# Performance work log

Measured on AMD Instinct MI355X. Metric: run time of the kernel, lower is better.

The kernel has to match this reference:

```python
import jax, jax.numpy as jnp
import numpy as np


def _gru_cell(x, h, W_ih, W_hh, b_ih, b_hh):
    # PyTorch GRUCell math, gate order (r, z, n) along the 3*H axis.
    gi = x @ W_ih.T + b_ih          # [B, 3H]
    gh = h @ W_hh.T + b_hh          # [B, 3H]
    i_r, i_z, i_n = jnp.split(gi, 3, axis=-1)
    h_r, h_z, h_n = jnp.split(gh, 3, axis=-1)
    r = jax.nn.sigmoid(i_r + h_r)
    z = jax.nn.sigmoid(i_z + h_z)
    n = jnp.tanh(i_n + r * h_n)
    return (1.0 - z) * n + z * h


def setup_inputs() -> dict:
    key = jax.random.key(0)
    ks = jax.random.split(key, 12)
    V, E, H, L, B, T = 16000, 512, 1024, 2, 32, 64
    s = 0.05  # small init scale to keep gates unsaturated
    return {
        "hidden": jax.random.normal(ks[0], (L, B, H), jnp.float32),
        "embed": jax.random.normal(ks[1], (V, E), jnp.float32) * s,
        "W_ih0": jax.random.normal(ks[2], (3 * H, E), jnp.float32) * s,
        "W_hh0": jax.random.normal(ks[3], (3 * H, H), jnp.float32) * s,
        "b_ih0": jax.random.normal(ks[4], (3 * H,), jnp.float32) * s,
        "b_hh0": jax.random.normal(ks[5], (3 * H,), jnp.float32) * s,
        "W_ih1": jax.random.normal(ks[6], (3 * H, H), jnp.float32) * s,
        "W_hh1": jax.random.normal(ks[7], (3 * H, H), jnp.float32) * s,
        "b_ih1": jax.random.normal(ks[8], (3 * H,), jnp.float32) * s,
        "b_hh1": jax.random.normal(ks[9], (3 * H,), jnp.float32) * s,
        "W_out": jax.random.normal(ks[10], (V, H), jnp.float32) * s,
        "b_out": jax.random.normal(ks[11], (V,), jnp.float32) * s,
        "max_len": 64,
        "batch_size": 32,
    }


def reference(hidden, embed, W_ih0, W_hh0, b_ih0, b_hh0,
              W_ih1, W_hh1, b_ih1, b_hh1, W_out, b_out,
              max_len, batch_size):
    # target=None path: teacher_forcing_ratio forced to 0 -> greedy argmax decode.
    tok0 = jnp.zeros((batch_size,), jnp.int32)  # curr_token starts at zeros

    def step(carry, _):
        h, tok = carry                      # h: [2, B, H], tok: [B] int32
        x = embed[tok]                      # [B, E] embedding lookup
        h0 = _gru_cell(x, h[0], W_ih0, W_hh0, b_ih0, b_hh0)
        h1 = _gru_cell(h0, h[1], W_ih1, W_hh1, b_ih1, b_hh1)
        logits = h1 @ W_out.T + b_out       # [B, V]
        tok_next = jnp.argmax(logits, axis=1).astype(jnp.int32)
        return (jnp.stack([h0, h1]), tok_next), logits

    (_, _), outputs = jax.lax.scan(step, (hidden, tok0), None, length=max_len)
    return outputs  # [max_len, B, V]
```

## Files before the change

### kernel.cpp

```cpp
#include <hip/hip_runtime.h>
#include <stdint.h>

#define V_ 16000
#define E_ 512
#define H_ 1024
#define B_ 32
#define T_ 64
#define NG_ 3072
#define NR_ 6144
#define IHB_ 96
#define TPAD_ 8

typedef float f32x4 __attribute__((ext_vector_type(4)));
typedef unsigned long long u64;

__device__ __forceinline__ unsigned int fkey(float f) {
    unsigned int u = __float_as_uint(f);
    return (u & 0x80000000u) ? ~u : (u | 0x80000000u);
}

__global__ void init_kernel(const float* __restrict__ hidden,
                            float* __restrict__ h0, float* __restrict__ h1,
                            u64* __restrict__ tokpk) {
    int idx = blockIdx.x * blockDim.x + threadIdx.x;
    if (idx < B_ * H_) {
        h0[idx] = hidden[idx];
        h1[idx] = hidden[B_ * H_ + idx];
    }
    if (idx < T_ * B_ * TPAD_) tokpk[idx] = 0ull;
}

__device__ __forceinline__ void gemm_core(
    const float* wp, const float* ap,
    int nch, float* lds, int tid, float acc[4][4])
{
    const int k4s = tid & 15;
    const int r   = tid >> 4;
    const int dW  = (r << 6) + ((k4s ^ (r & 7)) << 2);
    const int ks   = tid >> 6;
    const int lane = tid & 63;
    const int vg = lane >> 3, bg = lane & 7;

    f32x4 tW = *(const f32x4*)(wp + (k4s << 2));
    f32x4 tA = *(const f32x4*)(ap + (k4s << 2));
    *(f32x4*)&lds[dW] = tW;
    *(f32x4*)&lds[2048 + dW] = tA;
    __syncthreads();

    int cur = 0;
    for (int c = 0; c < nch; c++) {
        if (c + 1 < nch) {
            const int nko = (c + 1) << 6;
            tW = *(const f32x4*)(wp + nko + (k4s << 2));
            tA = *(const f32x4*)(ap + nko + (k4s << 2));
        }
        const float* Wb = &lds[cur * 4096];
        const float* Ab = &lds[cur * 4096 + 2048];
        #pragma unroll
        for (int kk = 0; kk < 2; kk++) {
            const int k4 = ks * 2 + kk;
            f32x4 ww[4], ha[4];
            #pragma unroll
            for (int vi = 0; vi < 4; vi++)
                ww[vi] = *(const f32x4*)&Wb[((vg + 8*vi) << 6) + ((k4 ^ vg) << 2)];
            #pragma unroll
            for (int j = 0; j < 4; j++)
                ha[j] = *(const f32x4*)&Ab[((bg + 8*j) << 6) + ((k4 ^ bg) << 2)];
            #pragma unroll
            for (int vi = 0; vi < 4; vi++)
                #pragma unroll
                for (int j = 0; j < 4; j++)
                    acc[vi][j] += ww[vi].x*ha[j].x + ww[vi].y*ha[j].y
                                + ww[vi].z*ha[j].z + ww[vi].w*ha[j].w;
        }
        if (c + 1 < nch) {
            float* Wo = &lds[(cur ^ 1) * 4096];
            *(f32x4*)&Wo[dW] = tW;
            *(f32x4*)&Wo[2048 + dW] = tA;
        }
        __syncthreads();
        cur ^= 1;
    }
}

__device__ __forceinline__ void ks_reduce(float* lds, int tid,
                                          float acc[4][4], float tv[16])
{
    const int ks = tid >> 6, lane = tid & 63;
    float* dst = &lds[(ks * 64 + lane) * 17];
    #pragma unroll
    for (int vi = 0; vi < 4; vi++)
        #pragma unroll
        for (int j = 0; j < 4; j++) dst[vi*4 + j] = acc[vi][j];
    __syncthreads();
    if (tid < 64) {
        #pragma unroll
        for (int c = 0; c < 16; c++) {
            float s = 0.f;
            #pragma unroll
            for (int k = 0; k < 8; k++) s += lds[(k*64 + tid)*17 + c];
            tv[c] = s;
        }
    }
}

__global__ __launch_bounds__(512) void gemm_gru(
    const float* __restrict__ Wih, const float* __restrict__ Whh, int Kih,
    const float* __restrict__ xbase, int xld,
    const float* __restrict__ embed, const u64* __restrict__ tokprev,
    int t, int tmode,
    const float* __restrict__ hprev,
    float* __restrict__ gbuf)
{
    __shared__ float lds[8704];
    const int tid = threadIdx.x;
    const int blk = blockIdx.x;
    const int r = tid >> 4;

    const float *wp, *ap;
    int nch;
    if (blk < IHB_) {
        const int n0 = blk * 32;
        wp = Wih + (size_t)(n0 + r) * Kih;
        if (tmode) {
            int tok = 0;
            if (t > 0)
                tok = (int)(0xFFFFFFFFu -
                            (unsigned)(tokprev[(size_t)r * TPAD_] & 0xFFFFFFFFull));
            ap = embed + (size_t)tok * Kih;
        } else {
            ap = xbase + (size_t)r * xld;
        }
        nch = Kih >> 6;
    } else {
        const int n0 = (blk - IHB_) * 32;
        wp = Whh + (size_t)(n0 + r) * H_;
        ap = hprev + (size_t)r * H_;
        nch = H_ >> 6;
    }

    float acc[4][4] = {};
    gemm_core(wp, ap, nch, lds, tid, acc);
    float tv[16];
    ks_reduce(lds, tid, acc, tv);
    if (tid < 64) {
        const int vgr = tid >> 3, bgr = tid & 7;
        const int nout0 = blk * 32;
        #pragma unroll
        for (int vi = 0; vi < 4; vi++)
            #pragma unroll
            for (int j = 0; j < 4; j++)
                gbuf[(size_t)(bgr + 8*j) * NR_ + nout0 + vgr + 8*vi] = tv[vi*4+j];
    }
}

__global__ __launch_bounds__(256) void combine_kernel(
    const float* __restrict__ gbuf,
    const float* __restrict__ bih, const float* __restrict__ bhh,
    const float* __restrict__ hprev, float* __restrict__ hnew)
{
    const int idx = blockIdx.x * 256 + threadIdx.x;
    const int b = idx >> 10, i = idx & 1023;
    const float* gb = gbuf + (size_t)b * NR_;
    const float gir = gb[i],        giz = gb[H_ + i],        gin = gb[2*H_ + i];
    const float ghr = gb[NG_ + i],  ghz = gb[NG_ + H_ + i],  ghn = gb[NG_ + 2*H_ + i];
    const float Sr = gir + ghr + bih[i] + bhh[i];
    const float Sz = giz + ghz + bih[H_ + i] + bhh[H_ + i];
    const float rr = 1.f / (1.f + expf(-Sr));
    const float zz = 1.f / (1.f + expf(-Sz));
    const float nn = tanhf(gin + bih[2*H_ + i] + rr * (ghn + bhh[2*H_ + i]));
    const float hp = hprev[(size_t)b * H_ + i];
    hnew[(size_t)b * H_ + i] = (1.f - zz) * nn + zz * hp;
}

__global__ __launch_bounds__(512) void logits_kernel(
    const float* __restrict__ h1, const float* __restrict__ Wout,
    const float* __restrict__ bout, float* __restrict__ out_t,
    u64* __restrict__ tokpk_t)
{
    __shared__ float lds[10272];
    const int tid = threadIdx.x;
    const int r = tid >> 4;
    const int v0 = blockIdx.x * 32;
    const float* wp = Wout + (size_t)(v0 + r) * H_;
    const float* ap = h1 + (size_t)r * H_;

    float acc[4][4] = {};
    gemm_core(wp, ap, H_ >> 6, lds, tid, acc);
    float tv[16];
    ks_reduce(lds, tid, acc, tv);

    float* totl = lds + 8704;
    u64*   am   = (u64*)(lds + 8704 + 1056);
    if (tid < 64) {
        const int vgr = tid >> 3, bgr = tid & 7;
        #pragma unroll
        for (int vi = 0; vi < 4; vi++) {
            const float bo = bout[v0 + vgr + 8*vi];
            #pragma unroll
            for (int j = 0; j < 4; j++) tv[vi*4+j] += bo;
        }
        #pragma unroll
        for (int vi = 0; vi < 4; vi++)
            #pragma unroll
            for (int j = 0; j < 4; j++)
                totl[(bgr + 8*j) * 33 + vgr + 8*vi] = tv[vi*4+j];
        #pragma unroll
        for (int j = 0; j < 4; j++) {
            u64 best = 0ull;
            #pragma unroll
            for (int vi = 0; vi < 4; vi++) {
                const int v = v0 + vgr + 8*vi;
                u64 p = ((u64)fkey(tv[vi*4+j]) << 32)
                      | (u64)(0xFFFFFFFFu - (unsigned)v);
                best = p > best ? p : best;
            }
            am[(bgr + 8*j) * 8 + vgr] = best;
        }
    }
    __syncthreads();
    if (tid < 64) {
        const int b = tid >> 1, half = tid & 1;
        #pragma unroll
        for (int q = 0; q < 4; q++) {
            f32x4 o;
            o.x = totl[b*33 + half*16 + q*4 + 0];
            o.y = totl[b*33 + half*16 + q*4 + 1];
            o.z = totl[b*33 + half*16 + q*4 + 2];
            o.w = totl[b*33 + half*16 + q*4 + 3];
            __builtin_nontemporal_store(
                o, (f32x4*)(out_t + (size_t)b * V_ + v0 + half*16 + q*4));
        }
    }
    if (tid < 32) {
        u64 best = 0ull;
        #pragma unroll
        for (int q = 0; q < 8; q++) {
            u64 p = am[tid*8 + q];
            best = p > best ? p : best;
        }
        atomicMax(&tokpk_t[(size_t)tid * TPAD_], best);
    }
}

extern "C" void kernel_launch(void* const* d_in, const int* in_sizes, int n_in,
                              void* d_out, int out_size, void* d_ws, size_t ws_size,
                              hipStream_t stream) {
    const float* hidden = (const float*)d_in[0];
    const float* embed  = (const float*)d_in[1];
    const float* Wih0   = (const float*)d_in[2];
    const float* Whh0   = (const float*)d_in[3];
    const float* bih0   = (const float*)d_in[4];
    const float* bhh0   = (const float*)d_in[5];
    const float* Wih1   = (const float*)d_in[6];
    const float* Whh1   = (const float*)d_in[7];
    const float* bih1   = (const float*)d_in[8];
    const float* bhh1   = (const float*)d_in[9];
    const float* Wout   = (const float*)d_in[10];
    const float* bout   = (const float*)d_in[11];
    float* out = (float*)d_out;

    const int BH = B_ * H_;
    float* ws = (float*)d_ws;
    float* h0buf = ws;
    float* h1buf = ws + 2 * BH;
    float* gbuf  = ws + 4 * BH;
    u64* tokpk = (u64*)(ws + 4 * BH + B_ * NR_);

    init_kernel<<<128, 256, 0, stream>>>(hidden, h0buf, h1buf, tokpk);

    for (int t = 0; t < T_; t++) {
        const int rp = t & 1, wp = (t + 1) & 1;
        const u64* tokprev = tokpk + (size_t)(t > 0 ? t - 1 : 0) * B_ * TPAD_;

        gemm_gru<<<NR_ / 32, 512, 0, stream>>>(
            Wih0, Whh0, E_, nullptr, 0, embed, tokprev, t, 1,
            h0buf + (size_t)rp * BH, gbuf);
        combine_kernel<<<128, 256, 0, stream>>>(
            gbuf, bih0, bhh0, h0buf + (size_t)rp * BH, h0buf + (size_t)wp * BH);

        gemm_gru<<<NR_ / 32, 512, 0, stream>>>(
            Wih1, Whh1, H_, h0buf + (size_t)wp * BH, H_, embed, tokprev, 0,
            0, h1buf + (size_t)rp * BH, gbuf);
        combine_kernel<<<128, 256, 0, stream>>>(
            gbuf, bih1, bhh1, h1buf + (size_t)rp * BH, h1buf + (size_t)wp * BH);

        logits_kernel<<<V_ / 32, 512, 0, stream>>>(
            h1buf + (size_t)wp * BH, Wout, bout,
            out + (size_t)t * B_ * V_, tokpk + (size_t)t * B_ * TPAD_);
    }
}
```

Before: 4.360 ms.

## Split GRU gate GEMM K dimension across two block slices, deepen prefetch

The gate GEMM grid is doubled so each block handles half of the K dimension, writing partial sums to two gbuf slices that combine_kernel adds together. The point is more parallelism: only 192 blocks ran before on a GPU with many CUs. Separately, gemm_core now keeps two chunks in flight in registers ahead of the LDS double buffer, which hides more global-load latency. The costs are extra workspace, extra partial-sum traffic in combine, and higher register pressure.

```diff
diff --git a/kernel.cpp b/kernel.cpp
--- a/kernel.cpp
+++ b/kernel.cpp
@@ -9,6 +9,7 @@
 #define NG_ 3072
 #define NR_ 6144
 #define IHB_ 96
+#define TB_ 192
 #define TPAD_ 8
 
 typedef float f32x4 __attribute__((ext_vector_type(4)));
@@ -40,22 +41,18 @@
     const int ks   = tid >> 6;
     const int lane = tid & 63;
     const int vg = lane >> 3, bg = lane & 7;
-
-    f32x4 tW = *(const f32x4*)(wp + (k4s << 2));
-    f32x4 tA = *(const f32x4*)(ap + (k4s << 2));
-    *(f32x4*)&lds[dW] = tW;
-    *(f32x4*)&lds[2048 + dW] = tA;
-    __syncthreads();
-
-    int cur = 0;
-    for (int c = 0; c < nch; c++) {
-        if (c + 1 < nch) {
-            const int nko = (c + 1) << 6;
-            tW = *(const f32x4*)(wp + nko + (k4s << 2));
-            tA = *(const f32x4*)(ap + nko + (k4s << 2));
-        }
-        const float* Wb = &lds[cur * 4096];
-        const float* Ab = &lds[cur * 4096 + 2048];
+    float* lds0 = lds;
+    float* lds1 = lds + 4096;
+
+    auto ldW = [&](int c) { return *(const f32x4*)(wp + (c << 6) + (k4s << 2)); };
+    auto ldA = [&](int c) { return *(const f32x4*)(ap + (c << 6) + (k4s << 2)); };
+    auto stb = [&](float* b, f32x4 w, f32x4 a) {
+        *(f32x4*)&b[dW] = w;
+        *(f32x4*)&b[2048 + dW] = a;
+    };
+    auto compute = [&](const float* b) {
+        const float* Wb = b;
+        const float* Ab = b + 2048;
         #pragma unroll
         for (int kk = 0; kk < 2; kk++) {
             const int k4 = ks * 2 + kk;
@@ -73,13 +70,27 @@
                     acc[vi][j] += ww[vi].x*ha[j].x + ww[vi].y*ha[j].y
                                 + ww[vi].z*ha[j].z + ww[vi].w*ha[j].w;
         }
-        if (c + 1 < nch) {
-            float* Wo = &lds[(cur ^ 1) * 4096];
-            *(f32x4*)&Wo[dW] = tW;
-            *(f32x4*)&Wo[2048 + dW] = tA;
-        }
+    };
+
+    { f32x4 w0 = ldW(0), a0 = ldA(0); stb(lds0, w0, a0); }
+    f32x4 wA = ldW(1), aA = ldA(1);
+    f32x4 wB = ldW(2), aB = ldA(2);
+    __syncthreads();
+
+    for (int c = 0; c < nch; c += 2) {
+        f32x4 wN = wA, aN = aA;
+        if (c + 3 < nch) { wN = ldW(c + 3); aN = ldA(c + 3); }
+        compute(lds0);
+        if (c + 1 < nch) stb(lds1, wA, aA);
         __syncthreads();
-        cur ^= 1;
+        if (c + 1 >= nch) break;
+        wA = wN; aA = aN;
+        f32x4 wM = wB, aM = aB;
+        if (c + 4 < nch) { wM = ldW(c + 4); aM = ldA(c + 4); }
+        compute(lds1);
+        if (c + 2 < nch) stb(lds0, wB, aB);
+        __syncthreads();
+        wB = wM; aB = aM;
     }
 }
 
@@ -114,11 +125,13 @@
 {
     __shared__ float lds[8704];
     const int tid = threadIdx.x;
-    const int blk = blockIdx.x;
+    const int blk0 = blockIdx.x;
+    const int kslice = blk0 >= TB_ ? 1 : 0;
+    const int blk = blk0 - kslice * TB_;
     const int r = tid >> 4;
 
     const float *wp, *ap;
-    int nch;
+    int Kfull;
     if (blk < IHB_) {
         const int n0 = blk * 32;
         wp = Wih + (size_t)(n0 + r) * Kih;
@@ -131,26 +144,29 @@
         } else {
             ap = xbase + (size_t)r * xld;
         }
-        nch = Kih >> 6;
+        Kfull = Kih;
     } else {
         const int n0 = (blk - IHB_) * 32;
         wp = Whh + (size_t)(n0 + r) * H_;
         ap = hprev + (size_t)r * H_;
-        nch = H_ >> 6;
-    }
+        Kfull = H_;
+    }
+    const int koff = kslice * (Kfull >> 1);
+    const int nch  = Kfull >> 7;
 
     float acc[4][4] = {};
-    gemm_core(wp, ap, nch, lds, tid, acc);
+    gemm_core(wp + koff, ap + koff, nch, lds, tid, acc);
     float tv[16];
     ks_reduce(lds, tid, acc, tv);
     if (tid < 64) {
         const int vgr = tid >> 3, bgr = tid & 7;
         const int nout0 = blk * 32;
+        float* gout = gbuf + (size_t)kslice * B_ * NR_;
         #pragma unroll
         for (int vi = 0; vi < 4; vi++)
             #pragma unroll
             for (int j = 0; j < 4; j++)
-                gbuf[(size_t)(bgr + 8*j) * NR_ + nout0 + vgr + 8*vi] = tv[vi*4+j];
+                gout[(size_t)(bgr + 8*j) * NR_ + nout0 + vgr + 8*vi] = tv[vi*4+j];
     }
 }
 
@@ -161,9 +177,14 @@
 {
     const int idx = blockIdx.x * 256 + threadIdx.x;
     const int b = idx >> 10, i = idx & 1023;
-    const float* gb = gbuf + (size_t)b * NR_;
-    const float gir = gb[i],        giz = gb[H_ + i],        gin = gb[2*H_ + i];
-    const float ghr = gb[NG_ + i],  ghz = gb[NG_ + H_ + i],  ghn = gb[NG_ + 2*H_ + i];
+    const float* gb0 = gbuf + (size_t)b * NR_;
+    const float* gb1 = gbuf + (size_t)(B_ + b) * NR_;
+    const float gir = gb0[i]         + gb1[i];
+    const float giz = gb0[H_ + i]    + gb1[H_ + i];
+    const float gin = gb0[2*H_ + i]  + gb1[2*H_ + i];
+    const float ghr = gb0[NG_ + i]        + gb1[NG_ + i];
+    const float ghz = gb0[NG_ + H_ + i]   + gb1[NG_ + H_ + i];
+    const float ghn = gb0[NG_ + 2*H_ + i] + gb1[NG_ + 2*H_ + i];
     const float Sr = gir + ghr + bih[i] + bhh[i];
     const float Sz = giz + ghz + bih[H_ + i] + bhh[H_ + i];
     const float rr = 1.f / (1.f + expf(-Sr));
@@ -265,7 +286,7 @@
     float* h0buf = ws;
     float* h1buf = ws + 2 * BH;
     float* gbuf  = ws + 4 * BH;
-    u64* tokpk = (u64*)(ws + 4 * BH + B_ * NR_);
+    u64* tokpk = (u64*)(ws + 4 * BH + 2 * B_ * NR_);
 
     init_kernel<<<128, 256, 0, stream>>>(hidden, h0buf, h1buf, tokpk);
 
@@ -273,13 +294,13 @@
         const int rp = t & 1, wp = (t + 1) & 1;
         const u64* tokprev = tokpk + (size_t)(t > 0 ? t - 1 : 0) * B_ * TPAD_;
 
-        gemm_gru<<<NR_ / 32, 512, 0, stream>>>(
+        gemm_gru<<<2 * TB_, 512, 0, stream>>>(
             Wih0, Whh0, E_, nullptr, 0, embed, tokprev, t, 1,
             h0buf + (size_t)rp * BH, gbuf);
         combine_kernel<<<128, 256, 0, stream>>>(
             gbuf, bih0, bhh0, h0buf + (size_t)rp * BH, h0buf + (size_t)wp * BH);
 
-        gemm_gru<<<NR_ / 32, 512, 0, stream>>>(
+        gemm_gru<<<2 * TB_, 512, 0, stream>>>(
             Wih1, Whh1, H_, h0buf + (size_t)wp * BH, H_, embed, tokprev, 0,
             0, h1buf + (size_t)rp * BH, gbuf);
         combine_kernel<<<128, 256, 0, stream>>>(
```

Result: no change. 4.407 ms (+1.1%).

## Use 64x32 register tiles with split-K GRU GEMMs and fewer logits blocks

Applied to the files above, without the earlier changes.

Each thread's register tile grows from 4x4 to 8x8 outputs, and each block from 32 to 64 output rows, with 256 threads instead of 512. This gives more FMA work per LDS load and loads each weight row fewer times. The GRU gate GEMMs split K in halves across two block sets, writing partial sums that the combine kernel adds, so the block count stays at 192. The logits kernel now uses 250 blocks of 64 vocab rows with a vectorized epilogue. Costs are higher register pressure, fewer blocks than CUs for logits, and extra gbuf traffic from the split-K partials.

```diff
diff --git a/kernel.cpp b/kernel.cpp
--- a/kernel.cpp
+++ b/kernel.cpp
@@ -8,7 +8,6 @@
 #define T_ 64
 #define NG_ 3072
 #define NR_ 6144
-#define IHB_ 96
 #define TPAD_ 8
 
 typedef float f32x4 __attribute__((ext_vector_type(4)));
@@ -30,81 +29,102 @@
     if (idx < T_ * B_ * TPAD_) tokpk[idx] = 0ull;
 }
 
-__device__ __forceinline__ void gemm_core(
-    const float* wp, const float* ap,
-    int nch, float* lds, int tid, float acc[4][4])
-{
-    const int k4s = tid & 15;
-    const int r   = tid >> 4;
-    const int dW  = (r << 6) + ((k4s ^ (r & 7)) << 2);
-    const int ks   = tid >> 6;
-    const int lane = tid & 63;
-    const int vg = lane >> 3, bg = lane & 7;
-
-    f32x4 tW = *(const f32x4*)(wp + (k4s << 2));
-    f32x4 tA = *(const f32x4*)(ap + (k4s << 2));
-    *(f32x4*)&lds[dW] = tW;
-    *(f32x4*)&lds[2048 + dW] = tA;
+__device__ __forceinline__ void gemm_core64(
+    const float* wq0, const float* wq1, const float* wq2, const float* wq3,
+    const float* aq0, const float* aq1,
+    int dW0, int dW1, int dW2, int dW3, int dA0, int dA1,
+    int nch, float* lds, int tid, float acc[8][8])
+{
+    const int ks = tid >> 5, pos = tid & 31;
+    const int rg = pos >> 2, bgp = pos & 3;
+
+    f32x4 w0 = *(const f32x4*)wq0, w1 = *(const f32x4*)wq1;
+    f32x4 w2 = *(const f32x4*)wq2, w3 = *(const f32x4*)wq3;
+    f32x4 a0 = *(const f32x4*)aq0, a1 = *(const f32x4*)aq1;
+    *(f32x4*)&lds[dW0] = w0; *(f32x4*)&lds[dW1] = w1;
+    *(f32x4*)&lds[dW2] = w2; *(f32x4*)&lds[dW3] = w3;
+    *(f32x4*)&lds[dA0] = a0; *(f32x4*)&lds[dA1] = a1;
     __syncthreads();
 
     int cur = 0;
     for (int c = 0; c < nch; c++) {
         if (c + 1 < nch) {
-            const int nko = (c + 1) << 6;
-            tW = *(const f32x4*)(wp + nko + (k4s << 2));
-            tA = *(const f32x4*)(ap + nko + (k4s << 2));
-        }
-        const float* Wb = &lds[cur * 4096];
-        const float* Ab = &lds[cur * 4096 + 2048];
+            const int o = (c + 1) << 6;
+            w0 = *(const f32x4*)(wq0 + o); w1 = *(const f32x4*)(wq1 + o);
+            w2 = *(const f32x4*)(wq2 + o); w3 = *(const f32x4*)(wq3 + o);
+            a0 = *(const f32x4*)(aq0 + o); a1 = *(const f32x4*)(aq1 + o);
+        }
+        const float* Wb = &lds[cur * 6144];
+        const float* Ab = Wb + 4096;
         #pragma unroll
         for (int kk = 0; kk < 2; kk++) {
             const int k4 = ks * 2 + kk;
-            f32x4 ww[4], ha[4];
+            f32x4 ww[8], ha[8];
             #pragma unroll
-            for (int vi = 0; vi < 4; vi++)
-                ww[vi] = *(const f32x4*)&Wb[((vg + 8*vi) << 6) + ((k4 ^ vg) << 2)];
+            for (int vi = 0; vi < 8; vi++) {
+                const int row = rg + 8 * vi;
+                ww[vi] = *(const f32x4*)&Wb[(row << 6) + ((k4 ^ rg) << 2)];
+            }
             #pragma unroll
-            for (int j = 0; j < 4; j++)
-                ha[j] = *(const f32x4*)&Ab[((bg + 8*j) << 6) + ((k4 ^ bg) << 2)];
+            for (int j = 0; j < 8; j++) {
+                const int br = bgp + 4 * j;
+                ha[j] = *(const f32x4*)&Ab[(br << 6) + ((k4 ^ (br & 7)) << 2)];
+            }
             #pragma unroll
-            for (int vi = 0; vi < 4; vi++)
+            for (int vi = 0; vi < 8; vi++)
                 #pragma unroll
-                for (int j = 0; j < 4; j++)
+                for (int j = 0; j < 8; j++)
                     acc[vi][j] += ww[vi].x*ha[j].x + ww[vi].y*ha[j].y
                                 + ww[vi].z*ha[j].z + ww[vi].w*ha[j].w;
         }
         if (c + 1 < nch) {
-            float* Wo = &lds[(cur ^ 1) * 4096];
-            *(f32x4*)&Wo[dW] = tW;
-            *(f32x4*)&Wo[2048 + dW] = tA;
+            float* L = &lds[(cur ^ 1) * 6144];
+            *(f32x4*)&L[dW0] = w0; *(f32x4*)&L[dW1] = w1;
+            *(f32x4*)&L[dW2] = w2; *(f32x4*)&L[dW3] = w3;
+            *(f32x4*)&L[dA0] = a0; *(f32x4*)&L[dA1] = a1;
         }
         __syncthreads();
         cur ^= 1;
     }
 }
 
-__device__ __forceinline__ void ks_reduce(float* lds, int tid,
-                                          float acc[4][4], float tv[16])
-{
-    const int ks = tid >> 6, lane = tid & 63;
-    float* dst = &lds[(ks * 64 + lane) * 17];
+__device__ __forceinline__ void reduce_totl(float* lds, int tid, float acc[8][8])
+{
+    const int ks = tid >> 5, pos = tid & 31;
+    {
+        float* dst = &lds[(ks * 32 + pos) * 68];
+        #pragma unroll
+        for (int vi = 0; vi < 8; vi++) {
+            f32x4 p0 = {acc[vi][0], acc[vi][1], acc[vi][2], acc[vi][3]};
+            f32x4 p1 = {acc[vi][4], acc[vi][5], acc[vi][6], acc[vi][7]};
+            *(f32x4*)&dst[vi * 8]     = p0;
+            *(f32x4*)&dst[vi * 8 + 4] = p1;
+        }
+    }
+    __syncthreads();
+    const int vi2 = tid >> 5, pos2 = tid & 31;
+    f32x4 s0 = {0.f, 0.f, 0.f, 0.f}, s1 = {0.f, 0.f, 0.f, 0.f};
     #pragma unroll
-    for (int vi = 0; vi < 4; vi++)
-        #pragma unroll
-        for (int j = 0; j < 4; j++) dst[vi*4 + j] = acc[vi][j];
-    __syncthreads();
-    if (tid < 64) {
-        #pragma unroll
-        for (int c = 0; c < 16; c++) {
-            float s = 0.f;
-            #pragma unroll
-            for (int k = 0; k < 8; k++) s += lds[(k*64 + tid)*17 + c];
-            tv[c] = s;
-        }
-    }
-}
-
-__global__ __launch_bounds__(512) void gemm_gru(
+    for (int k = 0; k < 8; k++) {
+        const float* src = &lds[(k * 32 + pos2) * 68 + vi2 * 8];
+        s0 += *(const f32x4*)src;
+        s1 += *(const f32x4*)(src + 4);
+    }
+    __syncthreads();
+    const int row = (pos2 >> 2) + 8 * vi2;
+    const int bb  = pos2 & 3;
+    lds[(bb +  0) * 68 + row] = s0.x;
+    lds[(bb +  4) * 68 + row] = s0.y;
+    lds[(bb +  8) * 68 + row] = s0.z;
+    lds[(bb + 12) * 68 + row] = s0.w;
+    lds[(bb + 16) * 68 + row] = s1.x;
+    lds[(bb + 20) * 68 + row] = s1.y;
+    lds[(bb + 24) * 68 + row] = s1.z;
+    lds[(bb + 28) * 68 + row] = s1.w;
+    __syncthreads();
+}
+
+__global__ __launch_bounds__(256) void gemm_gru(
     const float* __restrict__ Wih, const float* __restrict__ Whh, int Kih,
     const float* __restrict__ xbase, int xld,
     const float* __restrict__ embed, const u64* __restrict__ tokprev,
@@ -112,45 +132,71 @@
     const float* __restrict__ hprev,
     float* __restrict__ gbuf)
 {
-    __shared__ float lds[8704];
+    __shared__ float lds[17408];
     const int tid = threadIdx.x;
-    const int blk = blockIdx.x;
-    const int r = tid >> 4;
-
-    const float *wp, *ap;
-    int nch;
-    if (blk < IHB_) {
-        const int n0 = blk * 32;
-        wp = Wih + (size_t)(n0 + r) * Kih;
+    const int blk0 = blockIdx.x;
+    const int kslice = blk0 >= 96 ? 1 : 0;
+    const int tile = blk0 - kslice * 96;
+    const int k4s = tid & 15;
+    const int rr  = tid >> 4;
+
+    const float* Wbase; int K, n0, nout;
+    const float *ar0, *ar1;
+    if (tile < 48) {
+        n0 = tile * 64; nout = n0; Wbase = Wih; K = Kih;
         if (tmode) {
-            int tok = 0;
-            if (t > 0)
-                tok = (int)(0xFFFFFFFFu -
-                            (unsigned)(tokprev[(size_t)r * TPAD_] & 0xFFFFFFFFull));
-            ap = embed + (size_t)tok * Kih;
+            int tok0 = 0, tok1 = 0;
+            if (t > 0) {
+                tok0 = (int)(0xFFFFFFFFu -
+                       (unsigned)(tokprev[(size_t)rr * TPAD_] & 0xFFFFFFFFull));
+                tok1 = (int)(0xFFFFFFFFu -
+                       (unsigned)(tokprev[(size_t)(rr + 16) * TPAD_] & 0xFFFFFFFFull));
+            }
+            ar0 = embed + (size_t)tok0 * Kih;
+            ar1 = embed + (size_t)tok1 * Kih;
         } else {
-            ap = xbase + (size_t)r * xld;
-        }
-        nch = Kih >> 6;
+            ar0 = xbase + (size_t)rr * xld;
+            ar1 = xbase + (size_t)(rr + 16) * xld;
+        }
     } else {
-        const int n0 = (blk - IHB_) * 32;
-        wp = Whh + (size_t)(n0 + r) * H_;
-        ap = hprev + (size_t)r * H_;
-        nch = H_ >> 6;
-    }
-
-    float acc[4][4] = {};
-    gemm_core(wp, ap, nch, lds, tid, acc);
-    float tv[16];
-    ks_reduce(lds, tid, acc, tv);
-    if (tid < 64) {
-        const int vgr = tid >> 3, bgr = tid & 7;
-        const int nout0 = blk * 32;
-        #pragma unroll
-        for (int vi = 0; vi < 4; vi++)
-            #pragma unroll
-            for (int j = 0; j < 4; j++)
-                gbuf[(size_t)(bgr + 8*j) * NR_ + nout0 + vgr + 8*vi] = tv[vi*4+j];
+        n0 = (tile - 48) * 64; nout = NG_ + n0; Wbase = Whh; K = H_;
+        ar0 = hprev + (size_t)rr * H_;
+        ar1 = hprev + (size_t)(rr + 16) * H_;
+    }
+    const int koff = kslice * (K >> 1);
+    const int nch  = K >> 7;
+
+    const float *wq0, *wq1, *wq2, *wq3;
+    int dW0, dW1, dW2, dW3;
+    {
+        const int r0 = rr, r1 = 16 + rr, r2 = 32 + rr, r3 = 48 + rr;
+        wq0 = Wbase + (size_t)(n0 + r0) * K + koff + k4s * 4;
+        wq1 = Wbase + (size_t)(n0 + r1) * K + koff + k4s * 4;
+        wq2 = Wbase + (size_t)(n0 + r2) * K + koff + k4s * 4;
+        wq3 = Wbase + (size_t)(n0 + r3) * K + koff + k4s * 4;
+        dW0 = (r0 << 6) + ((k4s ^ (r0 & 7)) << 2);
+        dW1 = (r1 << 6) + ((k4s ^ (r1 & 7)) << 2);
+        dW2 = (r2 << 6) + ((k4s ^ (r2 & 7)) << 2);
+        dW3 = (r3 << 6) + ((k4s ^ (r3 & 7)) << 2);
+    }
+    const float* aq0 = ar0 + koff + k4s * 4;
+    const float* aq1 = ar1 + koff + k4s * 4;
+    const int dA0 = 4096 + (rr << 6) + ((k4s ^ (rr & 7)) << 2);
+    const int dA1 = 4096 + ((rr + 16) << 6) + ((k4s ^ (rr & 7)) << 2);
+
+    float acc[8][8] = {};
+    gemm_core64(wq0, wq1, wq2, wq3, aq0, aq1,
+                dW0, dW1, dW2, dW3, dA0, dA1, nch, lds, tid, acc);
+    reduce_totl(lds, tid, acc);
+
+    {
+        const int b = tid >> 3, seg = tid & 7;
+        float* gout = gbuf + (size_t)kslice * B_ * NR_
+                    + (size_t)b * NR_ + nout + seg * 8;
+        f32x4 x0 = *(f32x4*)&lds[b * 68 + seg * 8];
+        f32x4 x1 = *(f32x4*)&lds[b * 68 + seg * 8 + 4];
+        *(f32x4*)gout = x0;
+        *(f32x4*)(gout + 4) = x1;
     }
 }
 
@@ -161,9 +207,14 @@
 {
     const int idx = blockIdx.x * 256 + threadIdx.x;
     const int b = idx >> 10, i = idx & 1023;
-    const float* gb = gbuf + (size_t)b * NR_;
-    const float gir = gb[i],        giz = gb[H_ + i],        gin = gb[2*H_ + i];
-    const float ghr = gb[NG_ + i],  ghz = gb[NG_ + H_ + i],  ghn = gb[NG_ + 2*H_ + i];
+    const float* gb0 = gbuf + (size_t)b * NR_;
+    const float* gb1 = gbuf + (size_t)(B_ + b) * NR_;
+    const float gir = gb0[i]         + gb1[i];
+    const float giz = gb0[H_ + i]    + gb1[H_ + i];
+    const float gin = gb0[2*H_ + i]  + gb1[2*H_ + i];
+    const float ghr = gb0[NG_ + i]        + gb1[NG_ + i];
+    const float ghz = gb0[NG_ + H_ + i]   + gb1[NG_ + H_ + i];
+    const float ghn = gb0[NG_ + 2*H_ + i] + gb1[NG_ + 2*H_ + i];
     const float Sr = gir + ghr + bih[i] + bhh[i];
     const float Sz = giz + ghz + bih[H_ + i] + bhh[H_ + i];
     const float rr = 1.f / (1.f + expf(-Sr));
@@ -173,70 +224,69 @@
     hnew[(size_t)b * H_ + i] = (1.f - zz) * nn + zz * hp;
 }
 
-__global__ __launch_bounds__(512) void logits_kernel(
+__global__ __launch_bounds__(256) void logits_kernel(
     const float* __restrict__ h1, const float* __restrict__ Wout,
     const float* __restrict__ bout, float* __restrict__ out_t,
     u64* __restrict__ tokpk_t)
 {
-    __shared__ float lds[10272];
+    __shared__ float lds[17408];
     const int tid = threadIdx.x;
-    const int r = tid >> 4;
-    const int v0 = blockIdx.x * 32;
-    const float* wp = Wout + (size_t)(v0 + r) * H_;
-    const float* ap = h1 + (size_t)r * H_;
-
-    float acc[4][4] = {};
-    gemm_core(wp, ap, H_ >> 6, lds, tid, acc);
-    float tv[16];
-    ks_reduce(lds, tid, acc, tv);
-
-    float* totl = lds + 8704;
-    u64*   am   = (u64*)(lds + 8704 + 1056);
-    if (tid < 64) {
-        const int vgr = tid >> 3, bgr = tid & 7;
+    const int v0 = blockIdx.x * 64;
+    const int k4s = tid & 15;
+    const int rr  = tid >> 4;
+
+    const float *wq0, *wq1, *wq2, *wq3;
+    int dW0, dW1, dW2, dW3;
+    {
+        const int r0 = rr, r1 = 16 + rr, r2 = 32 + rr, r3 = 48 + rr;
+        wq0 = Wout + (size_t)(v0 + r0) * H_ + k4s * 4;
+        wq1 = Wout + (size_t)(v0 + r1) * H_ + k4s * 4;
+        wq2 = Wout + (size_t)(v0 + r2) * H_ + k4s * 4;
+        wq3 = Wout + (size_t)(v0 + r3) * H_ + k4s * 4;
+        dW0 = (r0 << 6) + ((k4s ^ (r0 & 7)) << 2);
+        dW1 = (r1 << 6) + ((k4s ^ (r1 & 7)) << 2);
+        dW2 = (r2 << 6) + ((k4s ^ (r2 & 7)) << 2);
+        dW3 = (r3 << 6) + ((k4s ^ (r3 & 7)) << 2);
+    }
+    const float* aq0 = h1 + (size_t)rr * H_ + k4s * 4;
+    const float* aq1 = h1 + (size_t)(rr + 16) * H_ + k4s * 4;
+    const int dA0 = 4096 + (rr << 6) + ((k4s ^ (rr & 7)) << 2);
+    const int dA1 = 4096 + ((rr + 16) << 6) + ((k4s ^ (rr & 7)) << 2);
+
+    float acc[8][8] = {};
+    gemm_core64(wq0, wq1, wq2, wq3, aq0, aq1,
+                dW0, dW1, dW2, dW3, dA0, dA1, H_ >> 6, lds, tid, acc);
+    reduce_totl(lds, tid, acc);
+
+    u64* am = (u64*)(lds + 2176);
+    {
+        const int b = tid >> 3, seg = tid & 7;
+        f32x4 x0 = *(f32x4*)&lds[b * 68 + seg * 8];
+        f32x4 x1 = *(f32x4*)&lds[b * 68 + seg * 8 + 4];
+        f32x4 bo0 = *(const f32x4*)(bout + v0 + seg * 8);
+        f32x4 bo1 = *(const f32x4*)(bout + v0 + seg * 8 + 4);
+        x0 += bo0; x1 += bo1;
+        __builtin_nontemporal_store(
+            x0, (f32x4*)(out_t + (size_t)b * V_ + v0 + seg * 8));
+        __builtin_nontemporal_store(
+            x1, (f32x4*)(out_t + (size_t)b * V_ + v0 + seg * 8 + 4));
+        const int vb = v0 + seg * 8;
+        float vals[8] = {x0.x, x0.y, x0.z, x0.w, x1.x, x1.y, x1.z, x1.w};
+        u64 best = 0ull;
         #pragma unroll
-        for (int vi = 0; vi < 4; vi++) {
-            const float bo = bout[v0 + vgr + 8*vi];
-            #pragma unroll
-            for (int j = 0; j < 4; j++) tv[vi*4+j] += bo;
-        }
-        #pragma unroll
-        for (int vi = 0; vi < 4; vi++)
-            #pragma unroll
-            for (int j = 0; j < 4; j++)
-                totl[(bgr + 8*j) * 33 + vgr + 8*vi] = tv[vi*4+j];
-        #pragma unroll
-        for (int j = 0; j < 4; j++) {
-            u64 best = 0ull;
-            #pragma unroll
-            for (int vi = 0; vi < 4; vi++) {
-                const int v = v0 + vgr + 8*vi;
-                u64 p = ((u64)fkey(tv[vi*4+j]) << 32)
-                      | (u64)(0xFFFFFFFFu - (unsigned)v);
-                best = p > best ? p : best;
-            }
-            am[(bgr + 8*j) * 8 + vgr] = best;
-        }
-    }
-    __syncthreads();
-    if (tid < 64) {
-        const int b = tid >> 1, half = tid & 1;
-        #pragma unroll
-        for (int q = 0; q < 4; q++) {
-            f32x4 o;
-            o.x = totl[b*33 + half*16 + q*4 + 0];
-            o.y = totl[b*33 + half*16 + q*4 + 1];
-            o.z = totl[b*33 + half*16 + q*4 + 2];
-            o.w = totl[b*33 + half*16 + q*4 + 3];
-            __builtin_nontemporal_store(
-                o, (f32x4*)(out_t + (size_t)b * V_ + v0 + half*16 + q*4));
-        }
-    }
+        for (int i = 0; i < 8; i++) {
+            u64 p = ((u64)fkey(vals[i]) << 32)
+                  | (u64)(0xFFFFFFFFu - (unsigned)(vb + i));
+            best = p > best ? p : best;
+        }
+        am[b * 8 + seg] = best;
+    }
+    __syncthreads();
     if (tid < 32) {
         u64 best = 0ull;
         #pragma unroll
         for (int q = 0; q < 8; q++) {
-            u64 p = am[tid*8 + q];
+            u64 p = am[tid * 8 + q];
             best = p > best ? p : best;
         }
         atomicMax(&tokpk_t[(size_t)tid * TPAD_], best);
@@ -265,7 +315,7 @@
     float* h0buf = ws;
     float* h1buf = ws + 2 * BH;
     float* gbuf  = ws + 4 * BH;
-    u64* tokpk = (u64*)(ws + 4 * BH + B_ * NR_);
+    u64* tokpk = (u64*)(ws + 4 * BH + 2 * B_ * NR_);
 
     init_kernel<<<128, 256, 0, stream>>>(hidden, h0buf, h1buf, tokpk);
 
@@ -273,19 +323,19 @@
         const int rp = t & 1, wp = (t + 1) & 1;
         const u64* tokprev = tokpk + (size_t)(t > 0 ? t - 1 : 0) * B_ * TPAD_;
 
-        gemm_gru<<<NR_ / 32, 512, 0, stream>>>(
+        gemm_gru<<<192, 256, 0, stream>>>(
             Wih0, Whh0, E_, nullptr, 0, embed, tokprev, t, 1,
             h0buf + (size_t)rp * BH, gbuf);
         combine_kernel<<<128, 256, 0, stream>>>(
             gbuf, bih0, bhh0, h0buf + (size_t)rp * BH, h0buf + (size_t)wp * BH);
 
-        gemm_gru<<<NR_ / 32, 512, 0, stream>>>(
+        gemm_gru<<<192, 256, 0, stream>>>(
             Wih1, Whh1, H_, h0buf + (size_t)wp * BH, H_, embed, tokprev, 0,
             0, h1buf + (size_t)rp * BH, gbuf);
         combine_kernel<<<128, 256, 0, stream>>>(
             gbuf, bih1, bhh1, h1buf + (size_t)rp * BH, h1buf + (size_t)wp * BH);
 
-        logits_kernel<<<V_ / 32, 512, 0, stream>>>(
+        logits_kernel<<<250, 256, 0, stream>>>(
             h1buf + (size_t)wp * BH, Wout, bout,
             out + (size_t)t * B_ * V_, tokpk + (size_t)t * B_ * TPAD_);
     }
```

Measured after the change: 3.944 ms. 9.5% less time.
